# Optimization experiments

Measured on AMD Instinct MI355X. Metric: run time of the kernel, lower is better.

Reference implementation:

```python
import jax, jax.numpy as jnp
import numpy as np
import math

B, N, K = 16, 1024, 16
NODE_DIM, MSG = 32, 128
EDGE_DIM = 4
EIN = MSG + EDGE_DIM  # edge_input_dim = message_dim + edge_dim
EPS = 1e-8
PI = math.pi


def _knn(pts, k):
    # pairwise_distance_etaphi + topk(smallest) -> neighbor indices [B,N,K]
    eta, phi = pts[:, 0], pts[:, 1]                                  # [B,N]
    deta = eta[:, :, None] - eta[:, None, :]
    dphi = jnp.mod(phi[:, :, None] - phi[:, None, :] + PI, 2 * PI) - PI
    dist = deta ** 2 + dphi ** 2                                     # [B,N,N]
    _, idx = jax.lax.top_k(-dist, k)                                 # smallest-k, sorted
    return idx


def _gather(x, idx):
    # x: [B,C,N], idx: [B,N,K] -> neighbor features [B,C,N,K]
    return jnp.take_along_axis(x[:, :, None, :], idx[:, None, :, :], axis=3)


def _ptrapphi(x):
    px, py, pz, e = x[:, 0:1], x[:, 1:2], x[:, 2:3], x[:, 3:4]
    pt = jnp.sqrt(px ** 2 + py ** 2)
    rap = 0.5 * jnp.log1p(2.0 * pz / jnp.clip(e - pz, 1e-20))
    phi = jnp.arctan2(py, px)
    return pt, rap, phi


def _pairwise_lv_fts(xi, xj):
    # [lnkt, lnz, lndelta, lnm2] along channel dim
    pti, rapi, phii = _ptrapphi(xi)
    ptj, rapj, phij = _ptrapphi(xj)
    ptmin = jnp.minimum(pti, ptj)
    dphi = jnp.mod(phii - phij + PI, 2 * PI) - PI
    delta = jnp.sqrt((rapi - rapj) ** 2 + dphi ** 2)
    lndelta = jnp.log(jnp.clip(delta, EPS))
    lnkt = jnp.log(jnp.clip(ptmin * delta, EPS))
    lnz = jnp.log(jnp.clip(ptmin / jnp.clip(pti + ptj, EPS), EPS))
    xij = xi + xj
    m2 = jnp.clip(xij[:, 3:4] ** 2 - (xij[:, :3] ** 2).sum(1, keepdims=True), EPS)
    lnm2 = jnp.log(m2)
    return jnp.concatenate([lnkt, lnz, lndelta, lnm2], axis=1)


def _bn(x, s, b):
    # eval-mode BatchNorm folded into per-channel scale/bias
    sh = (1, -1) + (1,) * (x.ndim - 2)
    return x * s.reshape(sh) + b.reshape(sh)


def _conv1x1(w, x):
    return jnp.einsum('oc,bc...->bo...', w, x)


def setup_inputs():
    key = jax.random.key(0)
    ks = jax.random.split(key, 12)
    pts = jax.random.normal(ks[0], (B, 2, N), jnp.float32)
    fts = jax.random.normal(ks[1], (B, NODE_DIM, N), jnp.float32)
    p3 = jax.random.normal(ks[2], (B, 3, N), jnp.float32) * 5.0
    e = jnp.sqrt((p3 ** 2).sum(1, keepdims=True) + 0.5)  # physical 4-vectors (E > |p|)
    lvs = jnp.concatenate([p3, e], axis=1)
    mask = jax.random.bernoulli(ks[3], 0.9, (B, 1, N))
    w = lambda k, o, i: (jax.random.normal(k, (o, i), jnp.float32) / np.sqrt(i)).astype(jnp.float32)
    return dict(
        pts=pts, fts=fts, lvs=lvs, mask=mask,
        bn1_s=jnp.ones(NODE_DIM, jnp.float32), bn1_b=jnp.zeros(NODE_DIM, jnp.float32),
        w_node=w(ks[4], MSG // 2, NODE_DIM),
        bn2_s=jnp.ones(EIN, jnp.float32), bn2_b=jnp.zeros(EIN, jnp.float32),
        w_e1=w(ks[5], MSG, EIN),
        bn3_s=jnp.ones(MSG, jnp.float32), bn3_b=jnp.zeros(MSG, jnp.float32),
        w_e2=w(ks[6], MSG, MSG),
        se_w1=w(ks[7], MSG // 16, MSG),
        se_w2=w(ks[8], MSG, MSG // 16),
    )


def reference(pts, fts, lvs, mask, bn1_s, bn1_b, w_node, bn2_s, bn2_b, w_e1, bn3_s, bn3_b, w_e2, se_w1, se_w2):
    idx = _knn(pts, K)                                                  # [B,N,K]
    # node_encode: BN -> ReLU -> 1x1 conv (node_dim -> MSG//2)
    node = _conv1x1(w_node, jax.nn.relu(_bn(fts, bn1_s, bn1_b)))        # [B,MSG/2,N]
    node_ngb = _gather(node, idx)                                       # [B,MSG/2,N,K]
    node_ctr = jnp.broadcast_to(node[..., None], node_ngb.shape)
    lvs_ngb = _gather(lvs, idx)                                         # [B,4,N,K]
    lv_fts = _pairwise_lv_fts(jnp.broadcast_to(lvs[..., None], lvs_ngb.shape), lvs_ngb)
    mf = mask.astype(jnp.float32)
    valid = _gather(mf, idx) * mf[..., None]                            # [B,1,N,K]
    x = jnp.concatenate([node_ctr, node_ngb, lv_fts], axis=1)           # [B,EIN,N,K]
    # edge_mlp: BN-ReLU-Conv1x1 x2
    x = _conv1x1(w_e1, jax.nn.relu(_bn(x, bn2_s, bn2_b)))
    x = _conv1x1(w_e2, jax.nn.relu(_bn(x, bn3_s, bn3_b)))               # [B,MSG,N,K]
    # SqueezeAndExcitation2d over valid edges
    n = valid.sum((2, 3))
    n = jnp.where(n == 0, 1.0, n)                                       # [B,1]
    y = (x * valid).sum((2, 3)) / n                                     # [B,MSG]
    y = jax.nn.sigmoid(jax.nn.relu(y @ se_w1.T) @ se_w2.T)
    x = x * y[:, :, None, None]
    # masked mean aggregation over neighbors
    x = x * valid
    agg = x.sum(-1) / jnp.clip(valid.sum(-1), 1.0)                      # [B,MSG,N]
    return agg
```

## Files before the change

### kernel.cpp

```cpp
#include <hip/hip_runtime.h>
#include <hip/hip_bf16.h>
#include <math.h>

typedef unsigned short u16;
typedef unsigned long long u64;

#define BB 16
#define NN 1024
#define KK 16
#define MSG 128
#define EINC 132
#define EPSF 1e-8f
#define PIF 3.14159274101257324f
#define TWOPIF 6.28318548202514648f

__device__ __forceinline__ float bf2f(u16 u) {
    return __uint_as_float(((unsigned int)u) << 16);
}
__device__ __forceinline__ float ldf(const void* p, int i, int fdt) {
    return fdt ? ((const float*)p)[i] : bf2f(((const u16*)p)[i]);
}
__device__ __forceinline__ float4 ldf4(const void* p, int i, int fdt) {
    if (fdt) return ((const float4*)p)[i >> 2];
    ushort4 u = ((const ushort4*)p)[i >> 2];
    return make_float4(bf2f(u.x), bf2f(u.y), bf2f(u.z), bf2f(u.w));
}
__device__ __forceinline__ float maskval(const void* m, int i, int mode) {
    if (mode == 0) return bf2f(((const u16*)m)[i]);
    if (mode == 1) return ((const float*)m)[i];
    if (mode == 2) return ((const unsigned char*)m)[i] ? 1.f : 0.f;
    return ((const int*)m)[i] ? 1.f : 0.f;
}

__global__ void sniff_kernel(const unsigned int* __restrict__ bn1s,
                             const u16* __restrict__ mask,
                             int* __restrict__ ctl) {
    if (threadIdx.x == 0 && blockIdx.x == 0) {
        ctl[0] = (bn1s[0] == 0x3F800000u) ? 1 : 0;
        bool bf = false, f32 = false, i8 = false;
        for (int q = 0; q < 64; ++q) {
            u16 u = mask[q];
            if (u == 0x3F80u) { if ((q & 1) == 0) bf = true; else f32 = true; }
            if (u == 0x0101u) i8 = true;
        }
        ctl[1] = bf ? 0 : (f32 ? 1 : (i8 ? 2 : 3));
    }
}

__device__ __forceinline__ float wrap2pi(float dp) {
    if (dp >= TWOPIF) dp = __fsub_rn(dp, TWOPIF);
    if (dp < 0.f) dp = __fadd_rn(dp, TWOPIF);
    return dp;
}

__device__ __forceinline__ void sort16(u64* x) {
#pragma unroll
    for (int k = 2; k <= 16; k <<= 1)
#pragma unroll
        for (int j = k >> 1; j > 0; j >>= 1)
#pragma unroll
            for (int i = 0; i < 16; ++i) {
                int l = i ^ j;
                if (l > i) {
                    bool up = ((i & k) == 0);
                    bool lt = x[l] < x[i];
                    bool sw = up ? lt : !lt;
                    u64 a = sw ? x[l] : x[i];
                    u64 b = sw ? x[i] : x[l];
                    x[i] = a; x[l] = b;
                }
            }
}

__device__ __forceinline__ void merge16(u64* L, const u64* R) {
#pragma unroll
    for (int k = 0; k < 16; ++k) {
        u64 o = R[15 - k];
        L[k] = (o < L[k]) ? o : L[k];
    }
#pragma unroll
    for (int j = 8; j > 0; j >>= 1)
#pragma unroll
        for (int i = 0; i < 16; ++i) {
            int l = i ^ j;
            if (l > i) {
                bool sw = L[l] < L[i];
                u64 a = sw ? L[l] : L[i];
                u64 b = sw ? L[i] : L[l];
                L[i] = a; L[l] = b;
            }
        }
}

__global__ __launch_bounds__(256) void knn_kernel(const void* __restrict__ pts,
                                                  int* __restrict__ idx,
                                                  const int* __restrict__ ctl) {
    __shared__ __align__(16) float seL[16 * 68 + 4];
    __shared__ __align__(16) float spL[16 * 68 + 4];
    __shared__ float pdL[16 * 257];
    __shared__ u16   piL[16 * 257];
    int fdt = ctl[0];
    int blk = blockIdx.x;
    int b = blk >> 6;
    int ibase = (blk & 63) << 4;
    int t = threadIdx.x;
    int pb = b * 2 * NN;
    for (int j = t; j < NN; j += 256) {
        int a = (j >> 6) * 68 + (j & 63);
        seL[a] = ldf(pts, pb + j, fdt);
        spL[a] = ldf(pts, pb + NN + j, fdt);
    }
    __syncthreads();
    int p = t >> 4, s = t & 15;
    {
        int i = ibase + p;
        int ia = (i >> 6) * 68 + (i & 63);
        float ei = seL[ia], pii = spL[ia];
        u64 lst[16], grp[16];
#pragma unroll
        for (int g = 0; g < 4; ++g) {
            const float* sep = &seL[s * 68 + g * 16];
            const float* spp = &spL[s * 68 + g * 16];
            int jb = (s << 6) + (g << 4);
#pragma unroll
            for (int q4 = 0; q4 < 4; ++q4) {
                float4 e4 = *(const float4*)(sep + 4 * q4);
                float4 p4 = *(const float4*)(spp + 4 * q4);
                float ee[4] = { e4.x, e4.y, e4.z, e4.w };
                float pp[4] = { p4.x, p4.y, p4.z, p4.w };
#pragma unroll
                for (int q = 0; q < 4; ++q) {
                    float de = __fsub_rn(ei, ee[q]);
                    float dp = wrap2pi(__fadd_rn(__fsub_rn(pii, pp[q]), PIF));
                    float dphi = __fsub_rn(dp, PIF);
                    float cd = __fadd_rn(__fmul_rn(de, de), __fmul_rn(dphi, dphi));
                    grp[q4 * 4 + q] = ((u64)__float_as_uint(cd) << 10)
                                      | (unsigned)(jb + q4 * 4 + q);
                }
            }
            sort16(grp);
            if (g == 0) {
#pragma unroll
                for (int k = 0; k < 16; ++k) lst[k] = grp[k];
            } else {
                merge16(lst, grp);
            }
        }
        int base = p * 257 + s * 16;
#pragma unroll
        for (int k = 0; k < 16; ++k) {
            pdL[base + k] = __uint_as_float((unsigned)(lst[k] >> 10));
            piL[base + k] = (u16)(lst[k] & 1023u);
        }
    }
    for (int stg = 0; stg < 4; ++stg) {
        __syncthreads();
        int stride = 8 >> stg;
        if (s < stride) {
            int Lb = p * 257 + s * 16;
            int Rb = p * 257 + (s + stride) * 16;
            u64 L[16], R[16];
#pragma unroll
            for (int k = 0; k < 16; ++k)
                L[k] = ((u64)__float_as_uint(pdL[Lb + k]) << 10) | piL[Lb + k];
#pragma unroll
            for (int k = 0; k < 16; ++k)
                R[k] = ((u64)__float_as_uint(pdL[Rb + k]) << 10) | piL[Rb + k];
            merge16(L, R);
#pragma unroll
            for (int k = 0; k < 16; ++k) {
                pdL[Lb + k] = __uint_as_float((unsigned)(L[k] >> 10));
                piL[Lb + k] = (u16)(L[k] & 1023u);
            }
        }
    }
    __syncthreads();
    {
        int p2 = t >> 4, k2 = t & 15;
        idx[(b * NN + ibase + p2) * KK + k2] = (int)piL[p2 * 257 + k2];
    }
}

__global__ __launch_bounds__(256) void ab1_kernel(
    const void* __restrict__ fts, const void* __restrict__ lvs,
    const void* __restrict__ bn1_s, const void* __restrict__ bn1_b,
    const void* __restrict__ w_node,
    const void* __restrict__ bn2_s, const void* __restrict__ bn2_b,
    float* __restrict__ rAB, float* __restrict__ prpx,
    const int* __restrict__ ctl) {
    __shared__ __align__(16) float fL[32 * 36];
    __shared__ __align__(16) float wnL[64 * 36];
    __shared__ float s2L[128], b2L[128];
    int fdt = ctl[0];
    int blk = blockIdx.x;
    int b = blk >> 5;
    int ibase = (blk & 31) << 5;
    int t = threadIdx.x;
    {
        int c = t >> 3, q = t & 7;
        float s1c = ldf(bn1_s, c, fdt), b1c = ldf(bn1_b, c, fdt);
        float4 v = ldf4(fts, (b * 32 + c) * NN + ibase + q * 4, fdt);
        float vv[4] = { v.x, v.y, v.z, v.w };
#pragma unroll
        for (int j = 0; j < 4; ++j)
            fL[(q * 4 + j) * 36 + c] = fmaxf(vv[j] * s1c + b1c, 0.f);
    }
#pragma unroll
    for (int m = 0; m < 2; ++m) {
        int e = t * 2 + m;
        int o = e >> 3, q = e & 7;
        float4 w = ldf4(w_node, o * 32 + q * 4, fdt);
        float* d = &wnL[o * 36 + q * 4];
        d[0] = w.x; d[1] = w.y; d[2] = w.z; d[3] = w.w;
    }
    if (t < 128) { s2L[t] = ldf(bn2_s, t, fdt); b2L[t] = ldf(bn2_b, t, fdt); }
    if (t < 32) {
        int i = ibase + t;
        int lb = b * 4 * NN;
        float px = ldf(lvs, lb + i, fdt),          py = ldf(lvs, lb + NN + i, fdt);
        float pz = ldf(lvs, lb + 2 * NN + i, fdt), e  = ldf(lvs, lb + 3 * NN + i, fdt);
        float pt = sqrtf(px * px + py * py);
        float rr = 2.f * pz / fmaxf(e - pz, 1e-20f);
        rr = fmaxf(rr, -0.99999994f);
        float rap = 0.5f * log1pf(rr);
        float phi = atan2f(py, px);
        float* o = prpx + (size_t)(b * NN + i) * 8;
        o[0] = px; o[1] = py; o[2] = pz; o[3] = e;
        o[4] = pt; o[5] = rap; o[6] = phi; o[7] = 0.f;
    }
    __syncthreads();
    int p = t >> 3, og = t & 7;
    float fr[32];
#pragma unroll
    for (int cc = 0; cc < 32; cc += 4) {
        float4 v = *(const float4*)&fL[p * 36 + cc];
        fr[cc] = v.x; fr[cc + 1] = v.y; fr[cc + 2] = v.z; fr[cc + 3] = v.w;
    }
    float aa[8];
#pragma unroll
    for (int m = 0; m < 8; ++m) {
        int no = og * 8 + m;
        float a = 0.f;
#pragma unroll
        for (int cc = 0; cc < 32; cc += 4) {
            float4 w = *(const float4*)&wnL[no * 36 + cc];
            a += w.x * fr[cc] + w.y * fr[cc + 1] + w.z * fr[cc + 2] + w.w * fr[cc + 3];
        }
        aa[m] = a;
    }
    size_t base = (size_t)(b * NN + ibase + p) * 128 + og * 8;
    float lo[8], hi[8];
#pragma unroll
    for (int m = 0; m < 8; ++m) {
        int no = og * 8 + m;
        lo[m] = fmaxf(aa[m] * s2L[no] + b2L[no], 0.f);
        hi[m] = fmaxf(aa[m] * s2L[64 + no] + b2L[64 + no], 0.f);
    }
    *(float4*)(rAB + base)      = make_float4(lo[0], lo[1], lo[2], lo[3]);
    *(float4*)(rAB + base + 4)  = make_float4(lo[4], lo[5], lo[6], lo[7]);
    *(float4*)(rAB + base + 64) = make_float4(hi[0], hi[1], hi[2], hi[3]);
    *(float4*)(rAB + base + 68) = make_float4(hi[4], hi[5], hi[6], hi[7]);
}

__global__ __launch_bounds__(256) void ab2_kernel(
    const float* __restrict__ rAB, const void* __restrict__ w_e1,
    float* __restrict__ A, float* __restrict__ Bv,
    const int* __restrict__ ctl) {
    __shared__ float rT[64 * 68];
    __shared__ float wsh[2048];
    int fdt = ctl[0];
    int blk = blockIdx.x;
    int half = blk & 1;
    int pc = blk >> 1;
    int b = pc >> 4, i0 = (pc & 15) << 6;
    int t = threadIdx.x;
    {
        int r = t >> 2, q = t & 3;
        const float4* src = (const float4*)(rAB + (size_t)(b * NN + i0 + r) * 128
                                            + half * 64 + q * 16);
#pragma unroll
        for (int m = 0; m < 4; ++m) {
            float4 v = src[m];
            int c = q * 16 + 4 * m;
            rT[(c + 0) * 68 + r] = v.x; rT[(c + 1) * 68 + r] = v.y;
            rT[(c + 2) * 68 + r] = v.z; rT[(c + 3) * 68 + r] = v.w;
        }
    }
    float acc[8][4];
#pragma unroll
    for (int oi = 0; oi < 8; ++oi)
#pragma unroll
        for (int ci = 0; ci < 4; ++ci) acc[oi][ci] = 0.f;
    int og = t >> 4, cg = t & 15;
    for (int jt = 0; jt < 4; ++jt) {
        __syncthreads();
        {
            int o = t >> 1, jh = (t & 1) * 8;
            float4 wa = ldf4(w_e1, o * EINC + half * 64 + jt * 16 + jh, fdt);
            float4 wb = ldf4(w_e1, o * EINC + half * 64 + jt * 16 + jh + 4, fdt);
            wsh[(jh + 0) * 128 + o] = wa.x; wsh[(jh + 1) * 128 + o] = wa.y;
            wsh[(jh + 2) * 128 + o] = wa.z; wsh[(jh + 3) * 128 + o] = wa.w;
            wsh[(jh + 4) * 128 + o] = wb.x; wsh[(jh + 5) * 128 + o] = wb.y;
            wsh[(jh + 6) * 128 + o] = wb.z; wsh[(jh + 7) * 128 + o] = wb.w;
        }
        __syncthreads();
#pragma unroll
        for (int jj = 0; jj < 16; ++jj) {
            int c = jt * 16 + jj;
            float4 hv = *(const float4*)&rT[c * 68 + cg * 4];
            float4 w0 = *(const float4*)&wsh[jj * 128 + og * 8];
            float4 w1 = *(const float4*)&wsh[jj * 128 + og * 8 + 4];
            float wv[8] = { w0.x, w0.y, w0.z, w0.w, w1.x, w1.y, w1.z, w1.w };
            float hvv[4] = { hv.x, hv.y, hv.z, hv.w };
#pragma unroll
            for (int oi = 0; oi < 8; ++oi)
#pragma unroll
                for (int ci = 0; ci < 4; ++ci)
                    acc[oi][ci] += wv[oi] * hvv[ci];
        }
    }
    float* dst = half ? Bv : A;
#pragma unroll
    for (int ci = 0; ci < 4; ++ci) {
        size_t g = (size_t)(b * NN + i0 + cg * 4 + ci) * 128 + og * 8;
        *(float4*)(dst + g)     = make_float4(acc[0][ci], acc[1][ci], acc[2][ci], acc[3][ci]);
        *(float4*)(dst + g + 4) = make_float4(acc[4][ci], acc[5][ci], acc[6][ci], acc[7][ci]);
    }
}

__global__ __launch_bounds__(256) void edge_kernel(
    const void* __restrict__ mask, const int* __restrict__ idx,
    const float* __restrict__ A, const float* __restrict__ Bv,
    const float* __restrict__ prpx,
    const void* __restrict__ bn2_s, const void* __restrict__ bn2_b,
    const void* __restrict__ w_e1,
    const void* __restrict__ bn3_s, const void* __restrict__ bn3_b,
    float* __restrict__ Hs, float* __restrict__ cnt, const int* __restrict__ ctl) {
    __shared__ float rlvL[128 * 4];
    __shared__ float validL[128];
    __shared__ int   idxsL[128];
    int fdt = ctl[0], mmode = ctl[1];
    int blk = blockIdx.x;
    int b = blk >> 7;
    int pbase = (blk & 127) << 3;
    int t = threadIdx.x;

    if (t < 128) {
        int col = t, pt = col >> 4, k = col & 15;
        int i = pbase + pt;
        int jn = idx[(b * NN + i) * KK + k];
        idxsL[col] = jn;
        float mi = maskval(mask, b * NN + i, mmode);
        float mj = maskval(mask, b * NN + jn, mmode);
        validL[col] = (mi != 0.f && mj != 0.f) ? 1.f : 0.f;
        const float4* pc = (const float4*)(prpx + (size_t)(b * NN + i) * 8);
        const float4* pn = (const float4*)(prpx + (size_t)(b * NN + jn) * 8);
        float4 c0 = pc[0], c1 = pc[1], n0 = pn[0], n1 = pn[1];
        float ptmin = fminf(c1.x, n1.x);
        float dpr = (c1.z - n1.z) + PIF;
        float r = fmodf(dpr, TWOPIF);
        r = (r < 0.f) ? r + TWOPIF : r;
        float dphi = r - PIF;
        float dr = c1.y - n1.y;
        float delta = sqrtf(dr * dr + dphi * dphi);
        float lndelta = logf(fmaxf(delta, EPSF));
        float lnkt = logf(fmaxf(ptmin * delta, EPSF));
        float lnz = logf(fmaxf(ptmin / fmaxf(c1.x + n1.x, EPSF), EPSF));
        float sx = c0.x + n0.x, sy = c0.y + n0.y, sz = c0.z + n0.z, see = c0.w + n0.w;
        float m2 = fmaxf(see * see - (sx * sx + sy * sy + sz * sz), EPSF);
        float f4a[4] = { lnkt, lnz, lndelta, logf(m2) };
        float rv[4];
#pragma unroll
        for (int q = 0; q < 4; ++q)
            rv[q] = fmaxf(f4a[q] * ldf(bn2_s, MSG + q, fdt) + ldf(bn2_b, MSG + q, fdt), 0.f);
        *(float4*)&rlvL[col * 4] = make_float4(rv[0], rv[1], rv[2], rv[3]);
    }
    __syncthreads();
    int pt = t >> 5, cq = t & 31;
    int i = pbase + pt;
    int c0 = cq * 4;
    float4 a4 = *(const float4*)(A + (size_t)(b * NN + i) * 128 + c0);
    float4 s3 = ldf4(bn3_s, c0, fdt), b3 = ldf4(bn3_b, c0, fdt);
    float4 w0 = ldf4(w_e1, (c0 + 0) * EINC + 128, fdt);
    float4 w1 = ldf4(w_e1, (c0 + 1) * EINC + 128, fdt);
    float4 w2 = ldf4(w_e1, (c0 + 2) * EINC + 128, fdt);
    float4 w3 = ldf4(w_e1, (c0 + 3) * EINC + 128, fdt);
    float4 acc = make_float4(0.f, 0.f, 0.f, 0.f);
#pragma unroll
    for (int k = 0; k < 16; ++k) {
        int col = pt * 16 + k;
        int jn = idxsL[col];
        float vk = validL[col];
        float4 rl = *(const float4*)&rlvL[col * 4];
        float4 b4 = *(const float4*)(Bv + (size_t)(b * NN + jn) * 128 + c0);
        float e0 = a4.x + b4.x + w0.x * rl.x + w0.y * rl.y + w0.z * rl.z + w0.w * rl.w;
        float e1 = a4.y + b4.y + w1.x * rl.x + w1.y * rl.y + w1.z * rl.z + w1.w * rl.w;
        float e2 = a4.z + b4.z + w2.x * rl.x + w2.y * rl.y + w2.z * rl.z + w2.w * rl.w;
        float e3 = a4.w + b4.w + w3.x * rl.x + w3.y * rl.y + w3.z * rl.z + w3.w * rl.w;
        acc.x += vk * fmaxf(s3.x * e0 + b3.x, 0.f);
        acc.y += vk * fmaxf(s3.y * e1 + b3.y, 0.f);
        acc.z += vk * fmaxf(s3.z * e2 + b3.z, 0.f);
        acc.w += vk * fmaxf(s3.w * e3 + b3.w, 0.f);
    }
    *(float4*)(Hs + (size_t)(b * NN + i) * 128 + c0) = acc;
    if (t < 8) {
        float cs = 0.f;
#pragma unroll
        for (int k = 0; k < 16; ++k) cs += validL[t * 16 + k];
        cnt[b * NN + pbase + t] = cs;
    }
}

__global__ __launch_bounds__(128) void reduceTh_kernel(const float* __restrict__ Hs,
                                                       float* __restrict__ Thp) {
    int blk = blockIdx.x;
    int b = blk >> 4, ch = blk & 15;
    int t = threadIdx.x;
    const float* p = Hs + (size_t)(b * NN + ch * 64) * 128 + t;
    float a = 0.f;
    for (int ii = 0; ii < 64; ++ii) a += p[ii * 128];
    Thp[blk * 128 + t] = a;
}

__global__ __launch_bounds__(128) void se_kernel(const float* __restrict__ Thp,
                                                 const float* __restrict__ cnt,
                                                 const void* __restrict__ w_e2,
                                                 const void* __restrict__ se_w1,
                                                 const void* __restrict__ se_w2,
                                                 float* __restrict__ y,
                                                 const int* __restrict__ ctl) {
    int b = blockIdx.x, t = threadIdx.x;
    int fdt = ctl[0];
    __shared__ float ThL[128], ybar[MSG], hh[8], part[2];
    float a = 0.f;
    for (int m = t; m < NN; m += 128) a += cnt[b * NN + m];
#pragma unroll
    for (int off = 32; off; off >>= 1) a += __shfl_down(a, off, 64);
    if ((t & 63) == 0) part[t >> 6] = a;
    float tv = 0.f;
#pragma unroll
    for (int ch = 0; ch < 16; ++ch) tv += Thp[(b * 16 + ch) * 128 + t];
    ThL[t] = tv;
    __syncthreads();
    float n = part[0] + part[1];
    n = (n == 0.f) ? 1.f : n;
    float T = 0.f;
#pragma unroll
    for (int j4 = 0; j4 < 32; ++j4) {
        float4 w = ldf4(w_e2, t * MSG + j4 * 4, fdt);
        T += w.x * ThL[j4 * 4] + w.y * ThL[j4 * 4 + 1] +
             w.z * ThL[j4 * 4 + 2] + w.w * ThL[j4 * 4 + 3];
    }
    ybar[t] = T / n;
    __syncthreads();
    if (t < 8) {
        float s = 0.f;
        for (int c = 0; c < MSG; ++c) s += ybar[c] * ldf(se_w1, t * MSG + c, fdt);
        hh[t] = fmaxf(s, 0.f);
    }
    __syncthreads();
    float s = 0.f;
#pragma unroll
    for (int j = 0; j < 8; ++j) s += hh[j] * ldf(se_w2, t * 8 + j, fdt);
    y[b * MSG + t] = 1.f / (1.f + expf(-s));
}

__global__ __launch_bounds__(256) void fin_kernel(const float* __restrict__ Hs,
                                                  const float* __restrict__ cnt,
                                                  const float* __restrict__ y,
                                                  const void* __restrict__ w_e2,
                                                  void* __restrict__ out,
                                                  const int* __restrict__ ctl) {
    __shared__ float HsT[128 * 68];
    __shared__ float wsh[2048];
    __shared__ float yL[128], icL[64];
    int fdt = ctl[0];
    int blk = blockIdx.x;
    int b = blk >> 4, i0 = (blk & 15) << 6;
    int t = threadIdx.x;
    {
        int r = t >> 2, q4 = t & 3;
        const float4* src = (const float4*)(Hs + (size_t)(b * NN + i0 + r) * 128 + q4 * 32);
#pragma unroll
        for (int m = 0; m < 8; ++m) {
            float4 v = src[m];
            int j = q4 * 32 + 4 * m;
            HsT[(j + 0) * 68 + r] = v.x; HsT[(j + 1) * 68 + r] = v.y;
            HsT[(j + 2) * 68 + r] = v.z; HsT[(j + 3) * 68 + r] = v.w;
        }
    }
    if (t < 128) yL[t] = y[b * 128 + t];
    else if (t < 192) icL[t - 128] = 1.f / fmaxf(cnt[b * NN + i0 + (t - 128)], 1.f);
    float acc[8][4];
#pragma unroll
    for (int oi = 0; oi < 8; ++oi)
#pragma unroll
        for (int ci = 0; ci < 4; ++ci) acc[oi][ci] = 0.f;
    int og = t >> 4, cg = t & 15;
    for (int jt = 0; jt < 8; ++jt) {
        __syncthreads();
        {
            int o = t >> 1, jh = (t & 1) * 8;
            float4 wa = ldf4(w_e2, o * MSG + jt * 16 + jh, fdt);
            float4 wb = ldf4(w_e2, o * MSG + jt * 16 + jh + 4, fdt);
            wsh[(jh + 0) * 128 + o] = wa.x; wsh[(jh + 1) * 128 + o] = wa.y;
            wsh[(jh + 2) * 128 + o] = wa.z; wsh[(jh + 3) * 128 + o] = wa.w;
            wsh[(jh + 4) * 128 + o] = wb.x; wsh[(jh + 5) * 128 + o] = wb.y;
            wsh[(jh + 6) * 128 + o] = wb.z; wsh[(jh + 7) * 128 + o] = wb.w;
        }
        __syncthreads();
#pragma unroll
        for (int jj = 0; jj < 16; ++jj) {
            int j = jt * 16 + jj;
            float4 hv = *(const float4*)&HsT[j * 68 + cg * 4];
            float4 w0 = *(const float4*)&wsh[jj * 128 + og * 8];
            float4 w1 = *(const float4*)&wsh[jj * 128 + og * 8 + 4];
            float wv[8] = { w0.x, w0.y, w0.z, w0.w, w1.x, w1.y, w1.z, w1.w };
            float hvv[4] = { hv.x, hv.y, hv.z, hv.w };
#pragma unroll
            for (int oi = 0; oi < 8; ++oi)
#pragma unroll
                for (int ci = 0; ci < 4; ++ci)
                    acc[oi][ci] += wv[oi] * hvv[ci];
        }
    }
    float ic[4] = { icL[cg * 4], icL[cg * 4 + 1], icL[cg * 4 + 2], icL[cg * 4 + 3] };
#pragma unroll
    for (int oi = 0; oi < 8; ++oi) {
        int o = og * 8 + oi;
        float yv = yL[o];
        float4 r;
        r.x = acc[oi][0] * yv * ic[0];
        r.y = acc[oi][1] * yv * ic[1];
        r.z = acc[oi][2] * yv * ic[2];
        r.w = acc[oi][3] * yv * ic[3];
        size_t g = (size_t)(b * 128 + o) * 1024 + i0 + cg * 4;
        if (fdt) *(float4*)((float*)out + g) = r;
        else {
            __hip_bfloat16* ob = (__hip_bfloat16*)out + g;
            ob[0] = __float2bfloat16(r.x); ob[1] = __float2bfloat16(r.y);
            ob[2] = __float2bfloat16(r.z); ob[3] = __float2bfloat16(r.w);
        }
    }
}

extern "C" void kernel_launch(void* const* d_in, const int* in_sizes, int n_in,
                              void* d_out, int out_size, void* d_ws, size_t ws_size,
                              hipStream_t stream) {
    const void* pts   = d_in[0];
    const void* fts   = d_in[1];
    const void* lvs   = d_in[2];
    const void* mask  = d_in[3];
    const void* bn1_s = d_in[4];
    const void* bn1_b = d_in[5];
    const void* w_node= d_in[6];
    const void* bn2_s = d_in[7];
    const void* bn2_b = d_in[8];
    const void* w_e1  = d_in[9];
    const void* bn3_s = d_in[10];
    const void* bn3_b = d_in[11];
    const void* w_e2  = d_in[12];
    const void* se_w1 = d_in[13];
    const void* se_w2 = d_in[14];

    char* ws = (char*)d_ws;
    size_t off = 0;
    int*   idx   = (int*)(ws + off);   off += (size_t)BB * NN * KK * 4;
    float* A     = (float*)(ws + off); off += (size_t)BB * NN * 128 * 4;
    float* Bv    = (float*)(ws + off); off += (size_t)BB * NN * 128 * 4;
    float* prpx  = (float*)(ws + off); off += (size_t)BB * NN * 8 * 4;
    float* HsU   = (float*)(ws + off); off += (size_t)BB * NN * 128 * 4;
    float* cnt   = (float*)(ws + off); off += (size_t)BB * NN * 4;
    float* Thp   = (float*)(ws + off); off += (size_t)256 * 128 * 4;
    float* y     = (float*)(ws + off); off += (size_t)BB * 128 * 4;
    int*   ctl   = (int*)(ws + off);

    sniff_kernel<<<1, 64, 0, stream>>>((const unsigned int*)bn1_s, (const u16*)mask, ctl);
    knn_kernel<<<1024, 256, 0, stream>>>(pts, idx, ctl);
    ab1_kernel<<<512, 256, 0, stream>>>(fts, lvs, bn1_s, bn1_b, w_node,
                                        bn2_s, bn2_b, HsU, prpx, ctl);
    ab2_kernel<<<512, 256, 0, stream>>>(HsU, w_e1, A, Bv, ctl);
    edge_kernel<<<2048, 256, 0, stream>>>(mask, idx, A, Bv, prpx, bn2_s, bn2_b,
                                          w_e1, bn3_s, bn3_b, HsU, cnt, ctl);
    reduceTh_kernel<<<256, 128, 0, stream>>>(HsU, Thp);
    se_kernel<<<BB, 128, 0, stream>>>(Thp, cnt, w_e2, se_w1, se_w2, y, ctl);
    fin_kernel<<<256, 256, 0, stream>>>(HsU, cnt, y, w_e2, d_out, ctl);
}
```

Measured before the change: 208.3 us.

## Fuse node-MLP kernels, fold channel reduction into edge kernel, shuffle-based kNN merge

The kNN merge stages now exchange sorted lists between lanes with wavefront shuffles, replacing the shared-memory staging and barriers. ab1 and ab2 are fused into one ab kernel, so the intermediate rAB buffer no longer round-trips through global memory. The per-channel sums for squeeze-excitation are reduced inside edge_kernel, which drops the separate reduceTh kernel. se_kernel now sums 128 partials per batch instead of 16, and fin_kernel is split across two output halves to double the block count.

```diff
diff --git a/kernel.cpp b/kernel.cpp
--- a/kernel.cpp
+++ b/kernel.cpp
@@ -51,6 +51,12 @@
     if (dp >= TWOPIF) dp = __fsub_rn(dp, TWOPIF);
     if (dp < 0.f) dp = __fadd_rn(dp, TWOPIF);
     return dp;
+}
+
+__device__ __forceinline__ u64 shfl64(u64 v, int src) {
+    int lo = __shfl((int)(unsigned)(v & 0xffffffffu), src, 64);
+    int hi = __shfl((int)(unsigned)(v >> 32), src, 64);
+    return ((u64)(unsigned)hi << 32) | (unsigned)lo;
 }
 
 __device__ __forceinline__ void sort16(u64* x) {
@@ -97,8 +103,6 @@
                                                   const int* __restrict__ ctl) {
     __shared__ __align__(16) float seL[16 * 68 + 4];
     __shared__ __align__(16) float spL[16 * 68 + 4];
-    __shared__ float pdL[16 * 257];
-    __shared__ u16   piL[16 * 257];
     int fdt = ctl[0];
     int blk = blockIdx.x;
     int b = blk >> 6;
@@ -112,94 +116,80 @@
     }
     __syncthreads();
     int p = t >> 4, s = t & 15;
-    {
-        int i = ibase + p;
-        int ia = (i >> 6) * 68 + (i & 63);
-        float ei = seL[ia], pii = spL[ia];
-        u64 lst[16], grp[16];
-#pragma unroll
-        for (int g = 0; g < 4; ++g) {
-            const float* sep = &seL[s * 68 + g * 16];
-            const float* spp = &spL[s * 68 + g * 16];
-            int jb = (s << 6) + (g << 4);
-#pragma unroll
-            for (int q4 = 0; q4 < 4; ++q4) {
-                float4 e4 = *(const float4*)(sep + 4 * q4);
-                float4 p4 = *(const float4*)(spp + 4 * q4);
-                float ee[4] = { e4.x, e4.y, e4.z, e4.w };
-                float pp[4] = { p4.x, p4.y, p4.z, p4.w };
-#pragma unroll
-                for (int q = 0; q < 4; ++q) {
-                    float de = __fsub_rn(ei, ee[q]);
-                    float dp = wrap2pi(__fadd_rn(__fsub_rn(pii, pp[q]), PIF));
-                    float dphi = __fsub_rn(dp, PIF);
-                    float cd = __fadd_rn(__fmul_rn(de, de), __fmul_rn(dphi, dphi));
-                    grp[q4 * 4 + q] = ((u64)__float_as_uint(cd) << 10)
-                                      | (unsigned)(jb + q4 * 4 + q);
-                }
+    int i = ibase + p;
+    int ia = (i >> 6) * 68 + (i & 63);
+    float ei = seL[ia], pii = spL[ia];
+    u64 lst[16], grp[16];
+#pragma unroll
+    for (int g = 0; g < 4; ++g) {
+        const float* sep = &seL[s * 68 + g * 16];
+        const float* spp = &spL[s * 68 + g * 16];
+        int jb = (s << 6) + (g << 4);
+#pragma unroll
+        for (int q4 = 0; q4 < 4; ++q4) {
+            float4 e4 = *(const float4*)(sep + 4 * q4);
+            float4 p4 = *(const float4*)(spp + 4 * q4);
+            float ee[4] = { e4.x, e4.y, e4.z, e4.w };
+            float pp[4] = { p4.x, p4.y, p4.z, p4.w };
+#pragma unroll
+            for (int q = 0; q < 4; ++q) {
+                float de = __fsub_rn(ei, ee[q]);
+                float dp = wrap2pi(__fadd_rn(__fsub_rn(pii, pp[q]), PIF));
+                float dphi = __fsub_rn(dp, PIF);
+                float cd = __fadd_rn(__fmul_rn(de, de), __fmul_rn(dphi, dphi));
+                grp[q4 * 4 + q] = ((u64)__float_as_uint(cd) << 10)
+                                  | (unsigned)(jb + q4 * 4 + q);
             }
-            sort16(grp);
-            if (g == 0) {
-#pragma unroll
-                for (int k = 0; k < 16; ++k) lst[k] = grp[k];
-            } else {
-                merge16(lst, grp);
-            }
-        }
-        int base = p * 257 + s * 16;
-#pragma unroll
-        for (int k = 0; k < 16; ++k) {
-            pdL[base + k] = __uint_as_float((unsigned)(lst[k] >> 10));
-            piL[base + k] = (u16)(lst[k] & 1023u);
-        }
-    }
-    for (int stg = 0; stg < 4; ++stg) {
-        __syncthreads();
-        int stride = 8 >> stg;
-        if (s < stride) {
-            int Lb = p * 257 + s * 16;
-            int Rb = p * 257 + (s + stride) * 16;
-            u64 L[16], R[16];
-#pragma unroll
-            for (int k = 0; k < 16; ++k)
-                L[k] = ((u64)__float_as_uint(pdL[Lb + k]) << 10) | piL[Lb + k];
-#pragma unroll
-            for (int k = 0; k < 16; ++k)
-                R[k] = ((u64)__float_as_uint(pdL[Rb + k]) << 10) | piL[Rb + k];
-            merge16(L, R);
-#pragma unroll
-            for (int k = 0; k < 16; ++k) {
-                pdL[Lb + k] = __uint_as_float((unsigned)(L[k] >> 10));
-                piL[Lb + k] = (u16)(L[k] & 1023u);
-            }
-        }
-    }
-    __syncthreads();
-    {
-        int p2 = t >> 4, k2 = t & 15;
-        idx[(b * NN + ibase + p2) * KK + k2] = (int)piL[p2 * 257 + k2];
-    }
-}
-
-__global__ __launch_bounds__(256) void ab1_kernel(
+        }
+        sort16(grp);
+        if (g == 0) {
+#pragma unroll
+            for (int k = 0; k < 16; ++k) lst[k] = grp[k];
+        } else {
+            merge16(lst, grp);
+        }
+    }
+    int lane = t & 63;
+#pragma unroll
+    for (int stride = 8; stride > 0; stride >>= 1) {
+        int src = (lane & 48) | ((s + stride) & 15);
+        u64 R[16];
+#pragma unroll
+        for (int k = 0; k < 16; ++k) R[k] = shfl64(lst[k], src);
+        merge16(lst, R);
+    }
+    int base = lane & 48;
+    int myj = 0;
+#pragma unroll
+    for (int k = 0; k < 16; ++k) {
+        int v = __shfl((int)(unsigned)(lst[k] & 1023u), base, 64);
+        if (s == k) myj = v;
+    }
+    idx[(b * NN + ibase + p) * KK + s] = myj;
+}
+
+__global__ __launch_bounds__(256) void ab_kernel(
     const void* __restrict__ fts, const void* __restrict__ lvs,
     const void* __restrict__ bn1_s, const void* __restrict__ bn1_b,
     const void* __restrict__ w_node,
     const void* __restrict__ bn2_s, const void* __restrict__ bn2_b,
-    float* __restrict__ rAB, float* __restrict__ prpx,
+    const void* __restrict__ w_e1,
+    float* __restrict__ A, float* __restrict__ Bv, float* __restrict__ prpx,
     const int* __restrict__ ctl) {
     __shared__ __align__(16) float fL[32 * 36];
     __shared__ __align__(16) float wnL[64 * 36];
+    __shared__ float rTA[64 * 36], rTB[64 * 36];
+    __shared__ float wsh[16 * 128];
     __shared__ float s2L[128], b2L[128];
     int fdt = ctl[0];
     int blk = blockIdx.x;
     int b = blk >> 5;
-    int ibase = (blk & 31) << 5;
+    int i0 = (blk & 31) << 5;
     int t = threadIdx.x;
     {
         int c = t >> 3, q = t & 7;
         float s1c = ldf(bn1_s, c, fdt), b1c = ldf(bn1_b, c, fdt);
-        float4 v = ldf4(fts, (b * 32 + c) * NN + ibase + q * 4, fdt);
+        float4 v = ldf4(fts, (b * 32 + c) * NN + i0 + q * 4, fdt);
         float vv[4] = { v.x, v.y, v.z, v.w };
 #pragma unroll
         for (int j = 0; j < 4; ++j)
@@ -215,7 +205,7 @@
     }
     if (t < 128) { s2L[t] = ldf(bn2_s, t, fdt); b2L[t] = ldf(bn2_b, t, fdt); }
     if (t < 32) {
-        int i = ibase + t;
+        int i = i0 + t;
         int lb = b * 4 * NN;
         float px = ldf(lvs, lb + i, fdt),          py = ldf(lvs, lb + NN + i, fdt);
         float pz = ldf(lvs, lb + 2 * NN + i, fdt), e  = ldf(lvs, lb + 3 * NN + i, fdt);
@@ -229,102 +219,69 @@
         o[4] = pt; o[5] = rap; o[6] = phi; o[7] = 0.f;
     }
     __syncthreads();
-    int p = t >> 3, og = t & 7;
-    float fr[32];
-#pragma unroll
-    for (int cc = 0; cc < 32; cc += 4) {
-        float4 v = *(const float4*)&fL[p * 36 + cc];
-        fr[cc] = v.x; fr[cc + 1] = v.y; fr[cc + 2] = v.z; fr[cc + 3] = v.w;
-    }
-    float aa[8];
-#pragma unroll
-    for (int m = 0; m < 8; ++m) {
-        int no = og * 8 + m;
-        float a = 0.f;
+    {
+        int p = t >> 3, og = t & 7;
+        float fr[32];
 #pragma unroll
         for (int cc = 0; cc < 32; cc += 4) {
-            float4 w = *(const float4*)&wnL[no * 36 + cc];
-            a += w.x * fr[cc] + w.y * fr[cc + 1] + w.z * fr[cc + 2] + w.w * fr[cc + 3];
-        }
-        aa[m] = a;
-    }
-    size_t base = (size_t)(b * NN + ibase + p) * 128 + og * 8;
-    float lo[8], hi[8];
-#pragma unroll
-    for (int m = 0; m < 8; ++m) {
-        int no = og * 8 + m;
-        lo[m] = fmaxf(aa[m] * s2L[no] + b2L[no], 0.f);
-        hi[m] = fmaxf(aa[m] * s2L[64 + no] + b2L[64 + no], 0.f);
-    }
-    *(float4*)(rAB + base)      = make_float4(lo[0], lo[1], lo[2], lo[3]);
-    *(float4*)(rAB + base + 4)  = make_float4(lo[4], lo[5], lo[6], lo[7]);
-    *(float4*)(rAB + base + 64) = make_float4(hi[0], hi[1], hi[2], hi[3]);
-    *(float4*)(rAB + base + 68) = make_float4(hi[4], hi[5], hi[6], hi[7]);
-}
-
-__global__ __launch_bounds__(256) void ab2_kernel(
-    const float* __restrict__ rAB, const void* __restrict__ w_e1,
-    float* __restrict__ A, float* __restrict__ Bv,
-    const int* __restrict__ ctl) {
-    __shared__ float rT[64 * 68];
-    __shared__ float wsh[2048];
-    int fdt = ctl[0];
-    int blk = blockIdx.x;
-    int half = blk & 1;
-    int pc = blk >> 1;
-    int b = pc >> 4, i0 = (pc & 15) << 6;
-    int t = threadIdx.x;
-    {
-        int r = t >> 2, q = t & 3;
-        const float4* src = (const float4*)(rAB + (size_t)(b * NN + i0 + r) * 128
-                                            + half * 64 + q * 16);
-#pragma unroll
-        for (int m = 0; m < 4; ++m) {
-            float4 v = src[m];
-            int c = q * 16 + 4 * m;
-            rT[(c + 0) * 68 + r] = v.x; rT[(c + 1) * 68 + r] = v.y;
-            rT[(c + 2) * 68 + r] = v.z; rT[(c + 3) * 68 + r] = v.w;
-        }
-    }
-    float acc[8][4];
-#pragma unroll
-    for (int oi = 0; oi < 8; ++oi)
-#pragma unroll
-        for (int ci = 0; ci < 4; ++ci) acc[oi][ci] = 0.f;
-    int og = t >> 4, cg = t & 15;
-    for (int jt = 0; jt < 4; ++jt) {
+            float4 v = *(const float4*)&fL[p * 36 + cc];
+            fr[cc] = v.x; fr[cc + 1] = v.y; fr[cc + 2] = v.z; fr[cc + 3] = v.w;
+        }
+#pragma unroll
+        for (int m = 0; m < 8; ++m) {
+            int no = og * 8 + m;
+            float a = 0.f;
+#pragma unroll
+            for (int cc = 0; cc < 32; cc += 4) {
+                float4 w = *(const float4*)&wnL[no * 36 + cc];
+                a += w.x * fr[cc] + w.y * fr[cc + 1] + w.z * fr[cc + 2] + w.w * fr[cc + 3];
+            }
+            rTA[no * 36 + p] = fmaxf(a * s2L[no] + b2L[no], 0.f);
+            rTB[no * 36 + p] = fmaxf(a * s2L[64 + no] + b2L[64 + no], 0.f);
+        }
+    }
+    int og = t >> 3, cg = t & 7;
+#pragma unroll
+    for (int half = 0; half < 2; ++half) {
+        const float* rT = half ? rTB : rTA;
+        float acc[4][4];
+#pragma unroll
+        for (int oi = 0; oi < 4; ++oi)
+#pragma unroll
+            for (int ci = 0; ci < 4; ++ci) acc[oi][ci] = 0.f;
+        for (int jt = 0; jt < 4; ++jt) {
+            __syncthreads();
+            {
+                int o = t >> 1, jh = (t & 1) * 8;
+                float4 wa = ldf4(w_e1, o * EINC + half * 64 + jt * 16 + jh, fdt);
+                float4 wb = ldf4(w_e1, o * EINC + half * 64 + jt * 16 + jh + 4, fdt);
+                wsh[(jh + 0) * 128 + o] = wa.x; wsh[(jh + 1) * 128 + o] = wa.y;
+                wsh[(jh + 2) * 128 + o] = wa.z; wsh[(jh + 3) * 128 + o] = wa.w;
+                wsh[(jh + 4) * 128 + o] = wb.x; wsh[(jh + 5) * 128 + o] = wb.y;
+                wsh[(jh + 6) * 128 + o] = wb.z; wsh[(jh + 7) * 128 + o] = wb.w;
+            }
+            __syncthreads();
+#pragma unroll
+            for (int jj = 0; jj < 16; ++jj) {
+                int c = jt * 16 + jj;
+                float4 hv = *(const float4*)&rT[c * 36 + cg * 4];
+                float4 wv = *(const float4*)&wsh[jj * 128 + og * 4];
+                float wvv[4] = { wv.x, wv.y, wv.z, wv.w };
+                float hvv[4] = { hv.x, hv.y, hv.z, hv.w };
+#pragma unroll
+                for (int oi = 0; oi < 4; ++oi)
+#pragma unroll
+                    for (int ci = 0; ci < 4; ++ci)
+                        acc[oi][ci] += wvv[oi] * hvv[ci];
+            }
+        }
+        float* dst = half ? Bv : A;
+#pragma unroll
+        for (int ci = 0; ci < 4; ++ci) {
+            size_t g = (size_t)(b * NN + i0 + cg * 4 + ci) * 128 + og * 4;
+            *(float4*)(dst + g) = make_float4(acc[0][ci], acc[1][ci], acc[2][ci], acc[3][ci]);
+        }
         __syncthreads();
-        {
-            int o = t >> 1, jh = (t & 1) * 8;
-            float4 wa = ldf4(w_e1, o * EINC + half * 64 + jt * 16 + jh, fdt);
-            float4 wb = ldf4(w_e1, o * EINC + half * 64 + jt * 16 + jh + 4, fdt);
-            wsh[(jh + 0) * 128 + o] = wa.x; wsh[(jh + 1) * 128 + o] = wa.y;
-            wsh[(jh + 2) * 128 + o] = wa.z; wsh[(jh + 3) * 128 + o] = wa.w;
-            wsh[(jh + 4) * 128 + o] = wb.x; wsh[(jh + 5) * 128 + o] = wb.y;
-            wsh[(jh + 6) * 128 + o] = wb.z; wsh[(jh + 7) * 128 + o] = wb.w;
-        }
-        __syncthreads();
-#pragma unroll
-        for (int jj = 0; jj < 16; ++jj) {
-            int c = jt * 16 + jj;
-            float4 hv = *(const float4*)&rT[c * 68 + cg * 4];
-            float4 w0 = *(const float4*)&wsh[jj * 128 + og * 8];
-            float4 w1 = *(const float4*)&wsh[jj * 128 + og * 8 + 4];
-            float wv[8] = { w0.x, w0.y, w0.z, w0.w, w1.x, w1.y, w1.z, w1.w };
-            float hvv[4] = { hv.x, hv.y, hv.z, hv.w };
-#pragma unroll
-            for (int oi = 0; oi < 8; ++oi)
-#pragma unroll
-                for (int ci = 0; ci < 4; ++ci)
-                    acc[oi][ci] += wv[oi] * hvv[ci];
-        }
-    }
-    float* dst = half ? Bv : A;
-#pragma unroll
-    for (int ci = 0; ci < 4; ++ci) {
-        size_t g = (size_t)(b * NN + i0 + cg * 4 + ci) * 128 + og * 8;
-        *(float4*)(dst + g)     = make_float4(acc[0][ci], acc[1][ci], acc[2][ci], acc[3][ci]);
-        *(float4*)(dst + g + 4) = make_float4(acc[4][ci], acc[5][ci], acc[6][ci], acc[7][ci]);
     }
 }
 
@@ -335,10 +292,12 @@
     const void* __restrict__ bn2_s, const void* __restrict__ bn2_b,
     const void* __restrict__ w_e1,
     const void* __restrict__ bn3_s, const void* __restrict__ bn3_b,
-    float* __restrict__ Hs, float* __restrict__ cnt, const int* __restrict__ ctl) {
+    float* __restrict__ Hs, float* __restrict__ cnt, float* __restrict__ Thp,
+    const int* __restrict__ ctl) {
     __shared__ float rlvL[128 * 4];
     __shared__ float validL[128];
     __shared__ int   idxsL[128];
+    __shared__ float thL[128 * 5];
     int fdt = ctl[0], mmode = ctl[1];
     int blk = blockIdx.x;
     int b = blk >> 7;
@@ -403,23 +362,28 @@
         acc.w += vk * fmaxf(s3.w * e3 + b3.w, 0.f);
     }
     *(float4*)(Hs + (size_t)(b * NN + i) * 128 + c0) = acc;
+    float4 a2;
+    a2.x = acc.x + __shfl_down(acc.x, 32, 64);
+    a2.y = acc.y + __shfl_down(acc.y, 32, 64);
+    a2.z = acc.z + __shfl_down(acc.z, 32, 64);
+    a2.w = acc.w + __shfl_down(acc.w, 32, 64);
+    int wv_ = t >> 6;
+    if ((t & 63) < 32) {
+        thL[(cq * 4 + 0) * 5 + wv_] = a2.x;
+        thL[(cq * 4 + 1) * 5 + wv_] = a2.y;
+        thL[(cq * 4 + 2) * 5 + wv_] = a2.z;
+        thL[(cq * 4 + 3) * 5 + wv_] = a2.w;
+    }
     if (t < 8) {
         float cs = 0.f;
 #pragma unroll
         for (int k = 0; k < 16; ++k) cs += validL[t * 16 + k];
         cnt[b * NN + pbase + t] = cs;
     }
-}
-
-__global__ __launch_bounds__(128) void reduceTh_kernel(const float* __restrict__ Hs,
-                                                       float* __restrict__ Thp) {
-    int blk = blockIdx.x;
-    int b = blk >> 4, ch = blk & 15;
-    int t = threadIdx.x;
-    const float* p = Hs + (size_t)(b * NN + ch * 64) * 128 + t;
-    float a = 0.f;
-    for (int ii = 0; ii < 64; ++ii) a += p[ii * 128];
-    Thp[blk * 128 + t] = a;
+    __syncthreads();
+    if (t < 128)
+        Thp[(size_t)blk * 128 + t] = thL[t * 5 + 0] + thL[t * 5 + 1]
+                                   + thL[t * 5 + 2] + thL[t * 5 + 3];
 }
 
 __global__ __launch_bounds__(128) void se_kernel(const float* __restrict__ Thp,
@@ -438,8 +402,7 @@
     for (int off = 32; off; off >>= 1) a += __shfl_down(a, off, 64);
     if ((t & 63) == 0) part[t >> 6] = a;
     float tv = 0.f;
-#pragma unroll
-    for (int ch = 0; ch < 16; ++ch) tv += Thp[(b * 16 + ch) * 128 + t];
+    for (int p = 0; p < 128; ++p) tv += Thp[(size_t)(b * 128 + p) * 128 + t];
     ThL[t] = tv;
     __syncthreads();
     float n = part[0] + part[1];
@@ -472,11 +435,13 @@
                                                   void* __restrict__ out,
                                                   const int* __restrict__ ctl) {
     __shared__ float HsT[128 * 68];
-    __shared__ float wsh[2048];
-    __shared__ float yL[128], icL[64];
+    __shared__ float wsh[16 * 64];
+    __shared__ float yL[64], icL[64];
     int fdt = ctl[0];
     int blk = blockIdx.x;
-    int b = blk >> 4, i0 = (blk & 15) << 6;
+    int oh = blk & 1;
+    int pc = blk >> 1;
+    int b = pc >> 4, i0 = (pc & 15) << 6;
     int t = threadIdx.x;
     {
         int r = t >> 2, q4 = t & 3;
@@ -489,46 +454,42 @@
             HsT[(j + 2) * 68 + r] = v.z; HsT[(j + 3) * 68 + r] = v.w;
         }
     }
-    if (t < 128) yL[t] = y[b * 128 + t];
-    else if (t < 192) icL[t - 128] = 1.f / fmaxf(cnt[b * NN + i0 + (t - 128)], 1.f);
-    float acc[8][4];
-#pragma unroll
-    for (int oi = 0; oi < 8; ++oi)
+    if (t < 64) yL[t] = y[b * 128 + oh * 64 + t];
+    else if (t < 128) icL[t - 64] = 1.f / fmaxf(cnt[b * NN + i0 + (t - 64)], 1.f);
+    float acc[4][4];
+#pragma unroll
+    for (int oi = 0; oi < 4; ++oi)
 #pragma unroll
         for (int ci = 0; ci < 4; ++ci) acc[oi][ci] = 0.f;
     int og = t >> 4, cg = t & 15;
     for (int jt = 0; jt < 8; ++jt) {
         __syncthreads();
         {
-            int o = t >> 1, jh = (t & 1) * 8;
-            float4 wa = ldf4(w_e2, o * MSG + jt * 16 + jh, fdt);
-            float4 wb = ldf4(w_e2, o * MSG + jt * 16 + jh + 4, fdt);
-            wsh[(jh + 0) * 128 + o] = wa.x; wsh[(jh + 1) * 128 + o] = wa.y;
-            wsh[(jh + 2) * 128 + o] = wa.z; wsh[(jh + 3) * 128 + o] = wa.w;
-            wsh[(jh + 4) * 128 + o] = wb.x; wsh[(jh + 5) * 128 + o] = wb.y;
-            wsh[(jh + 6) * 128 + o] = wb.z; wsh[(jh + 7) * 128 + o] = wb.w;
+            int o = t >> 2, jh = (t & 3) * 4;
+            float4 wa = ldf4(w_e2, (oh * 64 + o) * MSG + jt * 16 + jh, fdt);
+            wsh[(jh + 0) * 64 + o] = wa.x; wsh[(jh + 1) * 64 + o] = wa.y;
+            wsh[(jh + 2) * 64 + o] = wa.z; wsh[(jh + 3) * 64 + o] = wa.w;
         }
         __syncthreads();
 #pragma unroll
         for (int jj = 0; jj < 16; ++jj) {
             int j = jt * 16 + jj;
             float4 hv = *(const float4*)&HsT[j * 68 + cg * 4];
-            float4 w0 = *(const float4*)&wsh[jj * 128 + og * 8];
-            float4 w1 = *(const float4*)&wsh[jj * 128 + og * 8 + 4];
-            float wv[8] = { w0.x, w0.y, w0.z, w0.w, w1.x, w1.y, w1.z, w1.w };
+            float4 wv = *(const float4*)&wsh[jj * 64 + og * 4];
+            float wvv[4] = { wv.x, wv.y, wv.z, wv.w };
             float hvv[4] = { hv.x, hv.y, hv.z, hv.w };
 #pragma unroll
-            for (int oi = 0; oi < 8; ++oi)
+            for (int oi = 0; oi < 4; ++oi)
 #pragma unroll
                 for (int ci = 0; ci < 4; ++ci)
-                    acc[oi][ci] += wv[oi] * hvv[ci];
+                    acc[oi][ci] += wvv[oi] * hvv[ci];
         }
     }
     float ic[4] = { icL[cg * 4], icL[cg * 4 + 1], icL[cg * 4 + 2], icL[cg * 4 + 3] };
 #pragma unroll
-    for (int oi = 0; oi < 8; ++oi) {
-        int o = og * 8 + oi;
-        float yv = yL[o];
+    for (int oi = 0; oi < 4; ++oi) {
+        int o = oh * 64 + og * 4 + oi;
+        float yv = yL[og * 4 + oi];
         float4 r;
         r.x = acc[oi][0] * yv * ic[0];
         r.y = acc[oi][1] * yv * ic[1];
@@ -569,20 +530,18 @@
     float* A     = (float*)(ws + off); off += (size_t)BB * NN * 128 * 4;
     float* Bv    = (float*)(ws + off); off += (size_t)BB * NN * 128 * 4;
     float* prpx  = (float*)(ws + off); off += (size_t)BB * NN * 8 * 4;
-    float* HsU   = (float*)(ws + off); off += (size_t)BB * NN * 128 * 4;
+    float* Hs    = (float*)(ws + off); off += (size_t)BB * NN * 128 * 4;
     float* cnt   = (float*)(ws + off); off += (size_t)BB * NN * 4;
-    float* Thp   = (float*)(ws + off); off += (size_t)256 * 128 * 4;
+    float* Thp   = (float*)(ws + off); off += (size_t)2048 * 128 * 4;
     float* y     = (float*)(ws + off); off += (size_t)BB * 128 * 4;
     int*   ctl   = (int*)(ws + off);
 
     sniff_kernel<<<1, 64, 0, stream>>>((const unsigned int*)bn1_s, (const u16*)mask, ctl);
     knn_kernel<<<1024, 256, 0, stream>>>(pts, idx, ctl);
-    ab1_kernel<<<512, 256, 0, stream>>>(fts, lvs, bn1_s, bn1_b, w_node,
-                                        bn2_s, bn2_b, HsU, prpx, ctl);
-    ab2_kernel<<<512, 256, 0, stream>>>(HsU, w_e1, A, Bv, ctl);
+    ab_kernel<<<512, 256, 0, stream>>>(fts, lvs, bn1_s, bn1_b, w_node,
+                                       bn2_s, bn2_b, w_e1, A, Bv, prpx, ctl);
     edge_kernel<<<2048, 256, 0, stream>>>(mask, idx, A, Bv, prpx, bn2_s, bn2_b,
-                                          w_e1, bn3_s, bn3_b, HsU, cnt, ctl);
-    reduceTh_kernel<<<256, 128, 0, stream>>>(HsU, Thp);
+                                          w_e1, bn3_s, bn3_b, Hs, cnt, Thp, ctl);
     se_kernel<<<BB, 128, 0, stream>>>(Thp, cnt, w_e2, se_w1, se_w2, y, ctl);
-    fin_kernel<<<256, 256, 0, stream>>>(HsU, cnt, y, w_e2, d_out, ctl);
-}
+    fin_kernel<<<512, 256, 0, stream>>>(Hs, cnt, y, w_e2, d_out, ctl);
+}
```

Result: slower. 268.9 us (+29.1%).
